# Kernel tuning notes

Hardware: AMD Instinct MI355X
Metric: run time of the kernel (lower is better)

The kernel has to match this reference:

```python
import jax, jax.numpy as jnp
import numpy as np


def setup_inputs() -> dict:
    key = jax.random.key(0)
    kq, kk, kv = jax.random.split(key, 3)
    B, N, D = 8, 4096, 128
    Q = jax.random.normal(kq, (B, N, D), dtype=jnp.float32)
    K = jax.random.normal(kk, (B, N, D), dtype=jnp.float32)
    V = jax.random.normal(kv, (B, N, D), dtype=jnp.float32)
    return {"Q": Q, "K": K, "V": V}


def reference(Q, K, V):
    # attention = Q @ K^T  -> [B, N, N]  (scale=None, mask=None path)
    attention = jnp.einsum('bnd,bmd->bnm', Q, K)
    attention = jax.nn.softmax(attention, axis=-1)
    # context = attention @ V -> [B, N, D]
    context = jnp.einsum('bnm,bmd->bnd', attention, V)
    return context
```

## Files before the change

### kernel.cpp

```cpp
#include <hip/hip_runtime.h>

#define NB 8
#define SEQ 4096
#define DIM 128
#define BQ 128
#define KVB 32
#define NTILES (SEQ / KVB)
#define RMAX 43
#define IMG_BYTES 16384
#define WS_NEED ((size_t)NB * NTILES * IMG_BYTES)
#define L2E 1.44269504088896f

typedef _Float16 f16x8 __attribute__((ext_vector_type(8)));
typedef __bf16 bf16x8 __attribute__((ext_vector_type(8)));
typedef float f32x4 __attribute__((ext_vector_type(4)));
typedef float f32x16 __attribute__((ext_vector_type(16)));

struct U4 { unsigned x, y, z, w; };

static __device__ __forceinline__ unsigned cvtpk_bf16(float a, float b) {
  unsigned d;
  asm("v_cvt_pk_bf16_f32 %0, %1, %2" : "=v"(d) : "v"(a), "v"(b));
  return d;
}

#define EXP2(x) __builtin_amdgcn_exp2f(x)

__global__ void prep_kv(const float* __restrict__ K, const float* __restrict__ V,
                        unsigned char* __restrict__ ws) {
  const int t = blockIdx.x;
  const int b = blockIdx.y;
  unsigned char* img = ws + ((size_t)b * NTILES + t) * IMG_BYTES;
  int4* kimg = (int4*)img;
  int4* vimg = (int4*)(img + 8192);
  const float* Kb = K + ((size_t)b * SEQ + t * KVB) * DIM;
  const float* Vb = V + ((size_t)b * SEQ + t * KVB) * DIM;
  const int tid = threadIdx.x;

#pragma unroll
  for (int p = 0; p < 2; ++p) {
    const int un = tid + 256 * p;
    const int kv = un >> 4;
    const int c = (un & 15) ^ (kv & 15);
    const int s = c >> 1, hh = c & 1;
    const float* src = Kb + (size_t)kv * DIM + 16 * s + 8 * hh;
    f16x8 hv;
#pragma unroll
    for (int j = 0; j < 8; ++j) hv[j] = (_Float16)src[j];
    kimg[un] = __builtin_bit_cast(int4, hv);
  }

#pragma unroll
  for (int p = 0; p < 2; ++p) {
    const int un = tid + 256 * p;
    const int rr = un >> 4;
    const int c = (un & 15) ^ (rr & 15);
    const int dhi = c >> 2, s2 = (c >> 1) & 1, hh = c & 1;
    const int d = 32 * dhi + rr;
    bf16x8 hv;
#pragma unroll
    for (int e = 0; e < 8; ++e) {
      const int kv = 16 * s2 + 4 * hh + (e & 3) + 8 * (e >> 2);
      hv[e] = (__bf16)Vb[(size_t)kv * DIM + d];
    }
    vimg[un] = __builtin_bit_cast(int4, hv);
  }
}

__global__ __launch_bounds__(768, 3)
void attn_fwd12(const float* __restrict__ Q, const unsigned char* __restrict__ ws,
                float* __restrict__ O) {
  __shared__ __align__(16) unsigned char smem[98304];

  const int tid = threadIdx.x;
  const int w = tid >> 6;
  const int g = w >> 2;
  const int wg = w & 3;
  const int l = tid & 63;
  const int l31 = l & 31;
  const int h = l >> 5;

  const int bid = blockIdx.x;
  const int b = bid & 7;
  const int qt = bid >> 3;
  const size_t base = (size_t)b * SEQ * DIM;
  const int qrow = qt * BQ + wg * 32 + l31;

  f16x8 qf[8];
  {
    const float* qp = Q + base + (size_t)qrow * DIM + 8 * h;
#pragma unroll
    for (int s = 0; s < 8; ++s) {
      f32x4 a = *(const f32x4*)(qp + 16 * s);
      f32x4 c = *(const f32x4*)(qp + 16 * s + 4);
      f16x8 hv;
#pragma unroll
      for (int j = 0; j < 4; ++j) {
        hv[j] = (_Float16)(a[j] * L2E);
        hv[j + 4] = (_Float16)(c[j] * L2E);
      }
      qf[s] = hv;
    }
  }

  f32x16 o[4];
#pragma unroll
  for (int j = 0; j < 4; ++j) {
#pragma unroll
    for (int r = 0; r < 16; ++r) o[j][r] = 0.f;
  }
  float ls = 0.f;

  unsigned char* mybuf = smem + g * 32768;
  const unsigned char* wsb = ws + (size_t)b * NTILES * IMG_BYTES;

  auto STAGE = [&](int t, int bufsel) {
    const unsigned char* src = wsb + (size_t)t * IMG_BYTES + wg * 4096 + l * 16;
    unsigned char* dst = mybuf + bufsel * 16384 + wg * 4096;
#pragma unroll
    for (int i2 = 0; i2 < 4; ++i2) {
      __builtin_amdgcn_global_load_lds(
          (const __attribute__((address_space(1))) unsigned int*)(src + i2 * 1024),
          (__attribute__((address_space(3))) unsigned int*)(dst + i2 * 1024),
          16, 0, 0);
    }
  };

  const int lbase = l31 * 256 + ((((l31 & 15)) << 4) ^ (h << 4));

  STAGE(g, 0);
  __syncthreads();

#pragma unroll 1
  for (int i = 0; i < RMAX; ++i) {
    const int cur = i & 1;
    const int tcur = 3 * i + g;
    const int tnext = 3 * (i + 1) + g;
    if (tnext < NTILES) STAGE(tnext, cur ^ 1);

    if (tcur < NTILES) {
      const unsigned char* bufp = mybuf + cur * 16384;

      f32x16 s;
#pragma unroll
      for (int r = 0; r < 16; ++r) s[r] = 0.f;
      __builtin_amdgcn_s_setprio(1);
#pragma unroll
      for (int s8 = 0; s8 < 8; ++s8) {
        f16x8 kf = *(const f16x8*)(bufp + (lbase ^ (s8 << 5)));
        s = __builtin_amdgcn_mfma_f32_32x32x16_f16(kf, qf[s8], s, 0, 0, 0);
      }
      __builtin_amdgcn_s_setprio(0);

      float a0 = 0.f, a1 = 0.f, a2 = 0.f, a3 = 0.f;
#pragma unroll
      for (int r = 0; r < 16; r += 4) {
        s[r + 0] = EXP2(s[r + 0]);
        s[r + 1] = EXP2(s[r + 1]);
        s[r + 2] = EXP2(s[r + 2]);
        s[r + 3] = EXP2(s[r + 3]);
        a0 += s[r + 0]; a1 += s[r + 1]; a2 += s[r + 2]; a3 += s[r + 3];
      }
      ls += (a0 + a1) + (a2 + a3);

      bf16x8 pb[2];
#pragma unroll
      for (int u = 0; u < 2; ++u) {
        U4 t0 = {cvtpk_bf16(s[8 * u + 0], s[8 * u + 1]),
                 cvtpk_bf16(s[8 * u + 2], s[8 * u + 3]),
                 cvtpk_bf16(s[8 * u + 4], s[8 * u + 5]),
                 cvtpk_bf16(s[8 * u + 6], s[8 * u + 7])};
        pb[u] = __builtin_bit_cast(bf16x8, t0);
      }

      __builtin_amdgcn_s_setprio(1);
#pragma unroll
      for (int s2 = 0; s2 < 2; ++s2) {
#pragma unroll
        for (int j = 0; j < 4; ++j) {
          bf16x8 vf = *(const bf16x8*)(bufp + 8192 +
                                       (lbase ^ (j << 6) ^ (s2 << 5)));
          o[j] = __builtin_amdgcn_mfma_f32_32x32x16_bf16(vf, pb[s2], o[j], 0, 0, 0);
        }
      }
      __builtin_amdgcn_s_setprio(0);
    }
    __syncthreads();
  }

  ls += __shfl_xor(ls, 32);

  int4* park = (int4*)(smem + wg * 16384);
  float* lsp = (float*)(smem + 65536);
  const int lsi = wg * 32 + l31;

  __syncthreads();
#pragma unroll 1
  for (int stage = 0; stage < 3; ++stage) {
    if (g == stage) {
      if (stage == 0) {
#pragma unroll
        for (int j = 0; j < 4; ++j) {
#pragma unroll
          for (int rq = 0; rq < 4; ++rq) {
            f32x4 part = {o[j][4 * rq + 0], o[j][4 * rq + 1],
                          o[j][4 * rq + 2], o[j][4 * rq + 3]};
            park[l * 16 + ((4 * j + rq) ^ (l & 7))] =
                __builtin_bit_cast(int4, part);
          }
        }
        if (h == 0) lsp[lsi] = ls;
      } else if (stage == 1) {
#pragma unroll
        for (int j = 0; j < 4; ++j) {
#pragma unroll
          for (int rq = 0; rq < 4; ++rq) {
            const int idx = l * 16 + ((4 * j + rq) ^ (l & 7));
            f32x4 acc = __builtin_bit_cast(f32x4, park[idx]);
#pragma unroll
            for (int r = 0; r < 4; ++r) acc[r] += o[j][4 * rq + r];
            park[idx] = __builtin_bit_cast(int4, acc);
          }
        }
        if (h == 0) lsp[lsi] += ls;
      } else {
        const float inv = 1.0f / (lsp[lsi] + ls);
        float* Ob = O + base + (size_t)qrow * DIM;
#pragma unroll
        for (int j = 0; j < 4; ++j) {
#pragma unroll
          for (int rq = 0; rq < 4; ++rq) {
            const f32x4 acc = __builtin_bit_cast(
                f32x4, park[l * 16 + ((4 * j + rq) ^ (l & 7))]);
            f32x4 res;
#pragma unroll
            for (int r = 0; r < 4; ++r)
              res[r] = (acc[r] + o[j][4 * rq + r]) * inv;
            *(f32x4*)(Ob + 32 * j + 8 * rq + 4 * h) = res;
          }
        }
      }
    }
    __syncthreads();
  }
}

extern "C" void kernel_launch(void* const* d_in, const int* in_sizes, int n_in,
                              void* d_out, int out_size, void* d_ws,
                              size_t ws_size, hipStream_t stream) {
  const float* Q = (const float*)d_in[0];
  const float* K = (const float*)d_in[1];
  const float* V = (const float*)d_in[2];
  float* Out = (float*)d_out;
  if (ws_size < WS_NEED) return;
  prep_kv<<<dim3(NTILES, NB), dim3(256), 0, stream>>>(K, V, (unsigned char*)d_ws);
  attn_fwd12<<<dim3(SEQ / BQ * NB), dim3(768), 0, stream>>>(
      Q, (const unsigned char*)d_ws, Out);
}
```

Baseline: 95.16 us.

## Software-pipeline QK^T of next tile with softmax and PV using triple-buffered LDS

Moves the K/V staging to a three-slot LDS ring per wave group, raising shared memory from 96KB to 144KB. The QK^T MFMAs for the next tile are issued before the exp/bf16 conversion and PV MFMAs of the current tile, using two alternating score registers. The loop is unrolled by two, and each round ends with a vmcnt wait plus a raw barrier instead of __syncthreads. The aim is to hide exp and conversion latency and the staging wait behind matrix work. In exchange it holds an extra 16-register accumulator live, which risks register pressure or spills, and it uses much more LDS.

Result: slower. 116.2 us (+22.2%).

```diff
diff --git a/kernel.cpp b/kernel.cpp
--- a/kernel.cpp
+++ b/kernel.cpp
@@ -68,9 +68,9 @@
 }
 
 __global__ __launch_bounds__(768, 3)
-void attn_fwd12(const float* __restrict__ Q, const unsigned char* __restrict__ ws,
+void attn_fwd13(const float* __restrict__ Q, const unsigned char* __restrict__ ws,
                 float* __restrict__ O) {
-  __shared__ __align__(16) unsigned char smem[98304];
+  __shared__ __align__(16) unsigned char smem[147456];
 
   const int tid = threadIdx.x;
   const int w = tid >> 6;
@@ -111,7 +111,7 @@
   }
   float ls = 0.f;
 
-  unsigned char* mybuf = smem + g * 32768;
+  unsigned char* mybuf = smem + g * 49152;
   const unsigned char* wsb = ws + (size_t)b * NTILES * IMG_BYTES;
 
   auto STAGE = [&](int t, int bufsel) {
@@ -128,48 +128,48 @@
 
   const int lbase = l31 * 256 + ((((l31 & 15)) << 4) ^ (h << 4));
 
-  STAGE(g, 0);
-  __syncthreads();
-
-#pragma unroll 1
-  for (int i = 0; i < RMAX; ++i) {
-    const int cur = i & 1;
-    const int tcur = 3 * i + g;
-    const int tnext = 3 * (i + 1) + g;
-    if (tnext < NTILES) STAGE(tnext, cur ^ 1);
-
-    if (tcur < NTILES) {
-      const unsigned char* bufp = mybuf + cur * 16384;
-
-      f32x16 s;
-#pragma unroll
-      for (int r = 0; r < 16; ++r) s[r] = 0.f;
-      __builtin_amdgcn_s_setprio(1);
-#pragma unroll
-      for (int s8 = 0; s8 < 8; ++s8) {
-        f16x8 kf = *(const f16x8*)(bufp + (lbase ^ (s8 << 5)));
-        s = __builtin_amdgcn_mfma_f32_32x32x16_f16(kf, qf[s8], s, 0, 0, 0);
-      }
-      __builtin_amdgcn_s_setprio(0);
+  auto QKT = [&](const unsigned char* bufp, f32x16& s) {
+#pragma unroll
+    for (int r = 0; r < 16; ++r) s[r] = 0.f;
+    __builtin_amdgcn_s_setprio(1);
+#pragma unroll
+    for (int s8 = 0; s8 < 8; ++s8) {
+      f16x8 kf = *(const f16x8*)(bufp + (lbase ^ (s8 << 5)));
+      s = __builtin_amdgcn_mfma_f32_32x32x16_f16(kf, qf[s8], s, 0, 0, 0);
+    }
+    __builtin_amdgcn_s_setprio(0);
+  };
+
+  auto ROUND = [&](int i, f32x16& sCur, f32x16& sNext) {
+    const int ts = 3 * (i + 2) + g;
+    if (ts < NTILES) STAGE(ts, (i + 2) % 3);
+
+    const int tn = 3 * (i + 1) + g;
+    if (tn < NTILES) QKT(mybuf + ((i + 1) % 3) * 16384, sNext);
+
+    const int tc = 3 * i + g;
+    if (tc < NTILES) {
+      const unsigned char* bufp = mybuf + (i % 3) * 16384;
 
       float a0 = 0.f, a1 = 0.f, a2 = 0.f, a3 = 0.f;
 #pragma unroll
       for (int r = 0; r < 16; r += 4) {
-        s[r + 0] = EXP2(s[r + 0]);
-        s[r + 1] = EXP2(s[r + 1]);
-        s[r + 2] = EXP2(s[r + 2]);
-        s[r + 3] = EXP2(s[r + 3]);
-        a0 += s[r + 0]; a1 += s[r + 1]; a2 += s[r + 2]; a3 += s[r + 3];
+        sCur[r + 0] = EXP2(sCur[r + 0]);
+        sCur[r + 1] = EXP2(sCur[r + 1]);
+        sCur[r + 2] = EXP2(sCur[r + 2]);
+        sCur[r + 3] = EXP2(sCur[r + 3]);
+        a0 += sCur[r + 0]; a1 += sCur[r + 1];
+        a2 += sCur[r + 2]; a3 += sCur[r + 3];
       }
       ls += (a0 + a1) + (a2 + a3);
 
       bf16x8 pb[2];
 #pragma unroll
       for (int u = 0; u < 2; ++u) {
-        U4 t0 = {cvtpk_bf16(s[8 * u + 0], s[8 * u + 1]),
-                 cvtpk_bf16(s[8 * u + 2], s[8 * u + 3]),
-                 cvtpk_bf16(s[8 * u + 4], s[8 * u + 5]),
-                 cvtpk_bf16(s[8 * u + 6], s[8 * u + 7])};
+        U4 t0 = {cvtpk_bf16(sCur[8 * u + 0], sCur[8 * u + 1]),
+                 cvtpk_bf16(sCur[8 * u + 2], sCur[8 * u + 3]),
+                 cvtpk_bf16(sCur[8 * u + 4], sCur[8 * u + 5]),
+                 cvtpk_bf16(sCur[8 * u + 6], sCur[8 * u + 7])};
         pb[u] = __builtin_bit_cast(bf16x8, t0);
       }
 
@@ -185,8 +185,29 @@
       }
       __builtin_amdgcn_s_setprio(0);
     }
-    __syncthreads();
-  }
+
+    if (i + 1 < RMAX) {
+      asm volatile("s_waitcnt vmcnt(0)" ::: "memory");
+      __builtin_amdgcn_s_barrier();
+      __builtin_amdgcn_sched_barrier(0);
+    }
+  };
+
+  STAGE(g, 0);
+  STAGE(3 + g, 1);
+  asm volatile("s_waitcnt vmcnt(0)" ::: "memory");
+  __builtin_amdgcn_s_barrier();
+  __builtin_amdgcn_sched_barrier(0);
+
+  f32x16 sA, sB;
+  QKT(mybuf, sA);
+
+#pragma unroll 1
+  for (int i = 0; i + 1 < RMAX; i += 2) {
+    ROUND(i, sA, sB);
+    ROUND(i + 1, sB, sA);
+  }
+  ROUND(RMAX - 1, sA, sB);
 
   ls += __shfl_xor(ls, 32);
 
@@ -254,6 +275,6 @@
   float* Out = (float*)d_out;
   if (ws_size < WS_NEED) return;
   prep_kv<<<dim3(NTILES, NB), dim3(256), 0, stream>>>(K, V, (unsigned char*)d_ws);
-  attn_fwd12<<<dim3(SEQ / BQ * NB), dim3(768), 0, stream>>>(
+  attn_fwd13<<<dim3(SEQ / BQ * NB), dim3(768), 0, stream>>>(
       Q, (const unsigned char*)d_ws, Out);
 }
```
